# Kernel tuning notes

Hardware: AMD Instinct MI355X
Metric: run time of the kernel (lower is better)

## Reference

```python
import jax, jax.numpy as jnp
import numpy as np

N = 12288
IN_DIM = 256
OUT_DIM = 128
NEG_SLOPE = 0.01  # torch nn.LeakyReLU default


def setup_inputs() -> dict:
    key = jax.random.key(0)
    k1, k2, k3, k4, k5 = jax.random.split(key, 5)
    adj_mx = jax.random.randint(k1, (N, N), 0, 2, dtype=jnp.int32)
    input_features = jax.random.normal(k2, (N, IN_DIM), dtype=jnp.float32)
    # Linear(in_dim, out_dim): weight [out, in], bias [out]
    W = jax.random.normal(k3, (OUT_DIM, IN_DIM), dtype=jnp.float32) / np.sqrt(IN_DIM)
    b = jax.random.normal(k4, (OUT_DIM,), dtype=jnp.float32) * 0.01
    phi = jax.random.normal(k5, (2 * OUT_DIM, 1), dtype=jnp.float32)
    return {"adj_mx": adj_mx, "input_features": input_features, "W": W, "b": b, "phi": phi}


def reference(adj_mx, input_features, W, b, phi):
    # projection (dropout is identity in eval): [N, out]
    new_features = input_features @ W.T + b
    # additive attention halves: (N,1) + (1,N) -> [N,N]
    first_half = new_features @ phi[:OUT_DIM]          # [N,1]
    second_half = (new_features @ phi[OUT_DIM:]).T     # [1,N]
    similarity = jax.nn.leaky_relu(first_half + second_half, NEG_SLOPE)
    # adjacency with self-loops; mask non-edges to -1e20
    adj_hat = adj_mx.astype(jnp.float32) + jnp.eye(adj_mx.shape[0], dtype=jnp.float32)
    masked = jnp.where(adj_hat > 0, similarity, jnp.float32(-1e20))
    att = jax.nn.softmax(masked, axis=1)               # row-wise softmax [N,N]
    out = att @ new_features                           # [N, out]
    return jax.nn.leaky_relu(out, NEG_SLOPE)
```

## Files before the change

kernel.cpp:

```cpp
#include <hip/hip_runtime.h>
#include <hip/hip_bf16.h>

#define N_NODES 12288
#define IN_DIM 256
#define OUT_DIM 128
#define NEG 0.01f
#define LOG2E 1.44269504088896340736f
#define NSPLIT 4
#define JSPAN (N_NODES / NSPLIT)
#define TJ 64
#define NT (JSPAN / TJ)
#define VROW 68

typedef __attribute__((ext_vector_type(8))) short short8;
typedef __attribute__((ext_vector_type(4))) float f32x4;

__device__ __forceinline__ float fast_exp2(float x) {
#if __has_builtin(__builtin_amdgcn_exp2f)
  return __builtin_amdgcn_exp2f(x);
#else
  return exp2f(x);
#endif
}

__device__ __forceinline__ unsigned short f2bf(float x) {
  unsigned u = __float_as_uint(x);
  unsigned r = (u + 0x7FFFu + ((u >> 16) & 1u)) >> 16;
  return (unsigned short)r;
}

__global__ __launch_bounds__(256) void k1_proj(
    const float* __restrict__ X, const float* __restrict__ W,
    const float* __restrict__ bias, const float* __restrict__ phi,
    unsigned short* __restrict__ Vt, float* __restrict__ f,
    float* __restrict__ s, unsigned* __restrict__ smax) {
  __shared__ float Xs[32][40];
  __shared__ float Ws[32][136];
  __shared__ unsigned skey[8];
  const int t = threadIdx.x;
  const int i0 = blockIdx.x * 32;
  const int tx = t & 31, ty = t >> 5;
  float acc[4][4] = {};
  for (int k0 = 0; k0 < IN_DIM; k0 += 32) {
    __syncthreads();
    {
      int r = t >> 3, kq = (t & 7) * 4;
      float4 xv = *(const float4*)&X[(size_t)(i0 + r) * IN_DIM + k0 + kq];
      Xs[kq + 0][r] = xv.x; Xs[kq + 1][r] = xv.y;
      Xs[kq + 2][r] = xv.z; Xs[kq + 3][r] = xv.w;
    }
#pragma unroll
    for (int q = 0; q < 4; ++q) {
      int idx = t + q * 256;
      int c = idx >> 3, kq = (idx & 7) * 4;
      float4 wv = *(const float4*)&W[(size_t)c * IN_DIM + k0 + kq];
      Ws[kq + 0][c] = wv.x; Ws[kq + 1][c] = wv.y;
      Ws[kq + 2][c] = wv.z; Ws[kq + 3][c] = wv.w;
    }
    __syncthreads();
#pragma unroll
    for (int kk = 0; kk < 32; ++kk) {
      float4 a = *(const float4*)&Xs[kk][ty * 4];
      float4 bv = *(const float4*)&Ws[kk][tx * 4];
      float av[4] = {a.x, a.y, a.z, a.w};
      float bw[4] = {bv.x, bv.y, bv.z, bv.w};
#pragma unroll
      for (int r = 0; r < 4; ++r)
#pragma unroll
        for (int c = 0; c < 4; ++c) acc[r][c] += av[r] * bw[c];
    }
  }
  float4 bv = *(const float4*)&bias[tx * 4];
  float bb[4] = {bv.x, bv.y, bv.z, bv.w};
  float4 p1 = *(const float4*)&phi[tx * 4];
  float4 p2 = *(const float4*)&phi[OUT_DIM + tx * 4];
  float p1a[4] = {p1.x, p1.y, p1.z, p1.w};
  float p2a[4] = {p2.x, p2.y, p2.z, p2.w};
  float fp[4], sp_[4];
#pragma unroll
  for (int r = 0; r < 4; ++r) {
    int i = i0 + ty * 4 + r;
    float o[4];
    fp[r] = 0.f; sp_[r] = 0.f;
#pragma unroll
    for (int c = 0; c < 4; ++c) {
      o[c] = acc[r][c] + bb[c];
      Vt[(size_t)(tx * 4 + c) * N_NODES + i] = f2bf(o[c]);
      fp[r] = __builtin_fmaf(o[c], p1a[c], fp[r]);
      sp_[r] = __builtin_fmaf(o[c], p2a[c], sp_[r]);
    }
  }
#pragma unroll
  for (int o = 16; o; o >>= 1) {
#pragma unroll
    for (int r = 0; r < 4; ++r) {
      fp[r] += __shfl_xor(fp[r], o);
      sp_[r] += __shfl_xor(sp_[r], o);
    }
  }
  if (tx == 0) {
    unsigned kmax = 0;
#pragma unroll
    for (int r = 0; r < 4; ++r) {
      int i = i0 + ty * 4 + r;
      f[i] = fp[r]; s[i] = sp_[r];
      unsigned u = __float_as_uint(sp_[r]);
      unsigned key = (u & 0x80000000u) ? ~u : (u | 0x80000000u);
      kmax = max(kmax, key);
    }
    skey[ty] = kmax;
  }
  __syncthreads();
  if (t == 0) {
    unsigned kmax = skey[0];
#pragma unroll
    for (int q = 1; q < 8; ++q) kmax = max(kmax, skey[q]);
    atomicMax(smax, kmax);
  }
}

__global__ __launch_bounds__(256, 3) void k3_attn(
    const int* __restrict__ adj, const unsigned short* __restrict__ Vt,
    const float* __restrict__ f, const float* __restrict__ s,
    const unsigned* __restrict__ smaxk,
    float* __restrict__ pacc, float* __restrict__ pden) {
  __shared__ float s_lds[JSPAN];
  __shared__ __align__(16) unsigned short Vt_lds[2][128 * VROW];
  const int t = threadIdx.x;
  const int sp = blockIdx.x & (NSPLIT - 1);
  const int rb = blockIdx.x >> 2;
  const int j0g = sp * JSPAN;
  const int w = t >> 6, l = t & 63;
  const int m = l & 15, slot = l >> 4;
  const int row_g = rb * 64 + w * 16 + m;
#pragma unroll
  for (int q = 0; q < 3; ++q) {
    int idx = (t + q * 256) * 4;
    *(float4*)&s_lds[idx] = *(const float4*)&s[j0g + idx];
  }
  unsigned key = *smaxk;
  unsigned ku = (key & 0x80000000u) ? (key ^ 0x80000000u) : ~key;
  const float smaxv = __uint_as_float(ku);
  const float fi = f[row_g];
  const float xm = fi + smaxv;
  const float mrow = fmaxf(xm, NEG * xm);
  const float em = mrow * LOG2E;
  const int diag_g = row_g - j0g;
  float dsum = 0.f;
  f32x4 acc[8] = {};
  const int* adjp = adj + (size_t)row_g * N_NODES + j0g + 8 * slot;
  const int sd = t >> 1, sh = (t & 1) * 32;
  const unsigned short* vsrc = Vt + (size_t)sd * N_NODES + j0g + sh;
  unsigned short* vd0 = &Vt_lds[0][sd * VROW + sh];
  unsigned short* vd1 = &Vt_lds[1][sd * VROW + sh];
  int4 aA[4], aB[4], aC[4], vr[4];

#define ADJ_LOAD(SET, TT) { int _o = (TT) * TJ;                       \
    SET[0] = *(const int4*)(adjp + _o);                               \
    SET[1] = *(const int4*)(adjp + _o + 4);                           \
    SET[2] = *(const int4*)(adjp + _o + 32);                          \
    SET[3] = *(const int4*)(adjp + _o + 36); }
#define VT_LOAD(TT) { int _o = (TT) * TJ;                             \
    vr[0] = *(const int4*)(vsrc + _o);                                \
    vr[1] = *(const int4*)(vsrc + _o + 8);                            \
    vr[2] = *(const int4*)(vsrc + _o + 16);                           \
    vr[3] = *(const int4*)(vsrc + _o + 24); }
#define VT_WRITE(DST) { *(int4*)(DST) = vr[0]; *(int4*)((DST) + 8) = vr[1]; \
    *(int4*)((DST) + 16) = vr[2]; *(int4*)((DST) + 24) = vr[3]; }

  VT_LOAD(0);
  ADJ_LOAD(aA, 0);
  ADJ_LOAD(aB, 1);
  VT_WRITE(vd0);
  __syncthreads();
  int cur = 0;

#define ITER(TT, CURSET, PFSET) {                                           \
    int _tn = ((TT) + 1 < NT) ? (TT) + 1 : NT - 1;                          \
    VT_LOAD(_tn);                            \
    int _tp = ((TT) + 2 < NT) ? (TT) + 2 : NT - 1;                          \
    ADJ_LOAD(PFSET, _tp);                  \
    short8 af0, af1;                                                        \
    _Pragma("unroll")                                                       \
    for (int c = 0; c < 2; ++c) {                                           \
      int jb = (TT) * TJ + 32 * c + 8 * slot;                               \
      float4 sv0 = *(const float4*)&s_lds[jb];                              \
      float4 sv1 = *(const float4*)&s_lds[jb + 4];                          \
      int av[8] = {CURSET[2*c].x, CURSET[2*c].y, CURSET[2*c].z, CURSET[2*c].w, \
                   CURSET[2*c+1].x, CURSET[2*c+1].y, CURSET[2*c+1].z, CURSET[2*c+1].w}; \
      float sva[8] = {sv0.x, sv0.y, sv0.z, sv0.w, sv1.x, sv1.y, sv1.z, sv1.w}; \
      _Pragma("unroll")                                                     \
      for (int q = 0; q < 8; ++q) {                                         \
        float x = fi + sva[q];                                              \
        float xl = fmaxf(x, NEG * x);                                       \
        float e = fast_exp2(__builtin_fmaf(xl, LOG2E, -em));                \
        bool edge = (av[q] > 0) || ((jb + q) == diag_g);                    \
        float p = edge ? e : 0.f;                                           \
        dsum += p;                                                          \
        if (c == 0) af0[q] = (short)f2bf(p); else af1[q] = (short)f2bf(p);  \
      }                                                                     \
    }                                                                       \
    const unsigned short* vb = &Vt_lds[cur][0];                             \
    _Pragma("unroll")                                                       \
    for (int nt = 0; nt < 8; ++nt) {                                        \
      short8 b0 = *(const short8*)(vb + (nt * 16 + m) * VROW + 8 * slot);   \
      acc[nt] = __builtin_amdgcn_mfma_f32_16x16x32_bf16(af0, b0, acc[nt], 0, 0, 0); \
    }                                                                       \
    _Pragma("unroll")                                                       \
    for (int nt = 0; nt < 8; ++nt) {                                        \
      short8 b1 = *(const short8*)(vb + (nt * 16 + m) * VROW + 32 + 8 * slot); \
      acc[nt] = __builtin_amdgcn_mfma_f32_16x16x32_bf16(af1, b1, acc[nt], 0, 0, 0); \
    }                                                                       \
    unsigned short* vw = (cur ? vd0 : vd1);                                 \
    VT_WRITE(vw);                          \
    asm volatile("s_waitcnt lgkmcnt(0)" ::: "memory");                      \
    __builtin_amdgcn_sched_barrier(0);                                      \
    __builtin_amdgcn_s_barrier();                                           \
    cur ^= 1; }

  for (int tb = 0; tb < NT; tb += 3) {
    ITER(tb + 0, aA, aC);
    ITER(tb + 1, aB, aA);
    ITER(tb + 2, aC, aB);
  }
#undef ITER
#undef ADJ_LOAD
#undef VT_LOAD
#undef VT_WRITE

  dsum += __shfl_xor(dsum, 16);
  dsum += __shfl_xor(dsum, 32);
  if (l < 16) pden[sp * N_NODES + rb * 64 + w * 16 + l] = dsum;
  float* pa = pacc + (size_t)sp * N_NODES * OUT_DIM;
#pragma unroll
  for (int nt = 0; nt < 8; ++nt)
#pragma unroll
    for (int r = 0; r < 4; ++r) {
      int ii = rb * 64 + w * 16 + slot * 4 + r;
      pa[(size_t)ii * OUT_DIM + nt * 16 + m] = acc[nt][r];
    }
}

__global__ __launch_bounds__(256) void k4_comb(
    const float* __restrict__ pacc, const float* __restrict__ pden,
    float* __restrict__ out) {
  int idx = blockIdx.x * 256 + threadIdx.x;
  int i = idx >> 7;
  float v = 0.f, den = 0.f;
#pragma unroll
  for (int spp = 0; spp < NSPLIT; ++spp) {
    v += pacc[(size_t)spp * N_NODES * OUT_DIM + idx];
    den += pden[spp * N_NODES + i];
  }
  float o = v / den;
  out[idx] = fmaxf(o, NEG * o);
}

extern "C" void kernel_launch(void* const* d_in, const int* in_sizes, int n_in,
                              void* d_out, int out_size, void* d_ws, size_t ws_size,
                              hipStream_t stream) {
  const int* adj = (const int*)d_in[0];
  const float* X = (const float*)d_in[1];
  const float* W = (const float*)d_in[2];
  const float* b = (const float*)d_in[3];
  const float* phi = (const float*)d_in[4];
  float* out = (float*)d_out;
  char* ws = (char*)d_ws;
  unsigned short* Vt = (unsigned short*)(ws);
  float* fv   = (float*)(ws + 3145728);
  float* sv   = (float*)(ws + 3194880);
  unsigned* smax = (unsigned*)(ws + 3244032);
  float* pden = (float*)(ws + 3244048);
  float* pacc = (float*)(ws + 3440656);

  hipMemsetAsync(smax, 0, 4, stream);
  hipLaunchKernelGGL(k1_proj, dim3(N_NODES / 32), dim3(256), 0, stream,
                     X, W, b, phi, Vt, fv, sv, smax);
  hipLaunchKernelGGL(k3_attn, dim3((N_NODES / 64) * NSPLIT), dim3(256), 0, stream,
                     adj, Vt, fv, sv, smax, pacc, pden);
  hipLaunchKernelGGL(k4_comb, dim3((N_NODES * OUT_DIM) / 256), dim3(256), 0, stream,
                     pacc, pden, out);
}
```

Before: 990.9 us.

## Load V fragments directly from global memory, dropping LDS staging and barriers

The attention kernel no longer stages the transposed bf16 V tile through double-buffered LDS with per-tile barriers. Each wave now loads its MFMA B operands straight from global memory (relying on L2/L1 reuse across waves and blocks), and the adjacency prefetch is reduced to two register sets reloaded in place. Occupancy hint drops from 3 to 2 blocks per SM to leave room for the extra registers. This removes LDS traffic and synchronization, but every wave redundantly fetches V from cache with 16-byte strided accesses across rows, which can raise cache and memory pressure.

Result: slower. 1.024 ms (+3.3%).

```diff
diff --git a/kernel.cpp b/kernel.cpp
--- a/kernel.cpp
+++ b/kernel.cpp
@@ -10,10 +10,10 @@
 #define JSPAN (N_NODES / NSPLIT)
 #define TJ 64
 #define NT (JSPAN / TJ)
-#define VROW 68
 
 typedef __attribute__((ext_vector_type(8))) short short8;
 typedef __attribute__((ext_vector_type(4))) float f32x4;
+typedef __attribute__((ext_vector_type(4))) int i32x4;
 
 __device__ __forceinline__ float fast_exp2(float x) {
 #if __has_builtin(__builtin_amdgcn_exp2f)
@@ -119,13 +119,12 @@
   }
 }
 
-__global__ __launch_bounds__(256, 3) void k3_attn(
+__global__ __launch_bounds__(256, 2) void k3_attn(
     const int* __restrict__ adj, const unsigned short* __restrict__ Vt,
     const float* __restrict__ f, const float* __restrict__ s,
     const unsigned* __restrict__ smaxk,
     float* __restrict__ pacc, float* __restrict__ pden) {
   __shared__ float s_lds[JSPAN];
-  __shared__ __align__(16) unsigned short Vt_lds[2][128 * VROW];
   const int t = threadIdx.x;
   const int sp = blockIdx.x & (NSPLIT - 1);
   const int rb = blockIdx.x >> 2;
@@ -149,45 +148,35 @@
   float dsum = 0.f;
   f32x4 acc[8] = {};
   const int* adjp = adj + (size_t)row_g * N_NODES + j0g + 8 * slot;
-  const int sd = t >> 1, sh = (t & 1) * 32;
-  const unsigned short* vsrc = Vt + (size_t)sd * N_NODES + j0g + sh;
-  unsigned short* vd0 = &Vt_lds[0][sd * VROW + sh];
-  unsigned short* vd1 = &Vt_lds[1][sd * VROW + sh];
-  int4 aA[4], aB[4], aC[4], vr[4];
+  const unsigned short* vtp = Vt + (size_t)m * N_NODES + j0g + 8 * slot;
+  i32x4 aA[4], aB[4];
 
 #define ADJ_LOAD(SET, TT) { int _o = (TT) * TJ;                       \
-    SET[0] = *(const int4*)(adjp + _o);                               \
-    SET[1] = *(const int4*)(adjp + _o + 4);                           \
-    SET[2] = *(const int4*)(adjp + _o + 32);                          \
-    SET[3] = *(const int4*)(adjp + _o + 36); }
-#define VT_LOAD(TT) { int _o = (TT) * TJ;                             \
-    vr[0] = *(const int4*)(vsrc + _o);                                \
-    vr[1] = *(const int4*)(vsrc + _o + 8);                            \
-    vr[2] = *(const int4*)(vsrc + _o + 16);                           \
-    vr[3] = *(const int4*)(vsrc + _o + 24); }
-#define VT_WRITE(DST) { *(int4*)(DST) = vr[0]; *(int4*)((DST) + 8) = vr[1]; \
-    *(int4*)((DST) + 16) = vr[2]; *(int4*)((DST) + 24) = vr[3]; }
-
-  VT_LOAD(0);
+    SET[0] = *(const i32x4*)(adjp + _o);                              \
+    SET[1] = *(const i32x4*)(adjp + _o + 4);                          \
+    SET[2] = *(const i32x4*)(adjp + _o + 32);                         \
+    SET[3] = *(const i32x4*)(adjp + _o + 36); }
+
   ADJ_LOAD(aA, 0);
   ADJ_LOAD(aB, 1);
-  VT_WRITE(vd0);
   __syncthreads();
-  int cur = 0;
-
-#define ITER(TT, CURSET, PFSET) {                                           \
-    int _tn = ((TT) + 1 < NT) ? (TT) + 1 : NT - 1;                          \
-    VT_LOAD(_tn);                            \
-    int _tp = ((TT) + 2 < NT) ? (TT) + 2 : NT - 1;                          \
-    ADJ_LOAD(PFSET, _tp);                  \
+
+#define ITER(TT, SET) {                                                     \
+    short8 b0[8], b1[8];                                                    \
+    _Pragma("unroll")                                                       \
+    for (int nt = 0; nt < 8; ++nt)                                          \
+      b0[nt] = *(const short8*)(vtp + (size_t)nt * 16 * N_NODES + (TT) * TJ); \
+    _Pragma("unroll")                                                       \
+    for (int nt = 0; nt < 8; ++nt)                                          \
+      b1[nt] = *(const short8*)(vtp + (size_t)nt * 16 * N_NODES + (TT) * TJ + 32); \
     short8 af0, af1;                                                        \
     _Pragma("unroll")                                                       \
     for (int c = 0; c < 2; ++c) {                                           \
       int jb = (TT) * TJ + 32 * c + 8 * slot;                               \
       float4 sv0 = *(const float4*)&s_lds[jb];                              \
       float4 sv1 = *(const float4*)&s_lds[jb + 4];                          \
-      int av[8] = {CURSET[2*c].x, CURSET[2*c].y, CURSET[2*c].z, CURSET[2*c].w, \
-                   CURSET[2*c+1].x, CURSET[2*c+1].y, CURSET[2*c+1].z, CURSET[2*c+1].w}; \
+      int av[8] = {SET[2*c].x, SET[2*c].y, SET[2*c].z, SET[2*c].w,          \
+                   SET[2*c+1].x, SET[2*c+1].y, SET[2*c+1].z, SET[2*c+1].w}; \
       float sva[8] = {sv0.x, sv0.y, sv0.z, sv0.w, sv1.x, sv1.y, sv1.z, sv1.w}; \
       _Pragma("unroll")                                                     \
       for (int q = 0; q < 8; ++q) {                                         \
@@ -200,33 +189,21 @@
         if (c == 0) af0[q] = (short)f2bf(p); else af1[q] = (short)f2bf(p);  \
       }                                                                     \
     }                                                                       \
-    const unsigned short* vb = &Vt_lds[cur][0];                             \
-    _Pragma("unroll")                                                       \
-    for (int nt = 0; nt < 8; ++nt) {                                        \
-      short8 b0 = *(const short8*)(vb + (nt * 16 + m) * VROW + 8 * slot);   \
-      acc[nt] = __builtin_amdgcn_mfma_f32_16x16x32_bf16(af0, b0, acc[nt], 0, 0, 0); \
-    }                                                                       \
-    _Pragma("unroll")                                                       \
-    for (int nt = 0; nt < 8; ++nt) {                                        \
-      short8 b1 = *(const short8*)(vb + (nt * 16 + m) * VROW + 32 + 8 * slot); \
-      acc[nt] = __builtin_amdgcn_mfma_f32_16x16x32_bf16(af1, b1, acc[nt], 0, 0, 0); \
-    }                                                                       \
-    unsigned short* vw = (cur ? vd0 : vd1);                                 \
-    VT_WRITE(vw);                          \
-    asm volatile("s_waitcnt lgkmcnt(0)" ::: "memory");                      \
-    __builtin_amdgcn_sched_barrier(0);                                      \
-    __builtin_amdgcn_s_barrier();                                           \
-    cur ^= 1; }
-
-  for (int tb = 0; tb < NT; tb += 3) {
-    ITER(tb + 0, aA, aC);
-    ITER(tb + 1, aB, aA);
-    ITER(tb + 2, aC, aB);
+    ADJ_LOAD(SET, ((TT) + 2 < NT) ? (TT) + 2 : NT - 1);   \
+    _Pragma("unroll")                                                       \
+    for (int nt = 0; nt < 8; ++nt)                                          \
+      acc[nt] = __builtin_amdgcn_mfma_f32_16x16x32_bf16(af0, b0[nt], acc[nt], 0, 0, 0); \
+    _Pragma("unroll")                                                       \
+    for (int nt = 0; nt < 8; ++nt)                                          \
+      acc[nt] = __builtin_amdgcn_mfma_f32_16x16x32_bf16(af1, b1[nt], acc[nt], 0, 0, 0); \
+  }
+
+  for (int tb = 0; tb < NT; tb += 2) {
+    ITER(tb, aA);
+    ITER(tb + 1, aB);
   }
 #undef ITER
 #undef ADJ_LOAD
-#undef VT_LOAD
-#undef VT_WRITE
 
   dsum += __shfl_xor(dsum, 16);
   dsum += __shfl_xor(dsum, 32);
```
